# Optimization experiments

Measured on AMD Instinct MI355X. Metric: run time of the kernel, lower is better.

## Reference

```python
import jax, jax.numpy as jnp
import numpy as np

NUM_HEADS = 8
MASK_RATE = 0.5


def setup_inputs() -> dict:
    key = jax.random.key(0)
    ks = jax.random.split(key, 6)
    B, N, C = 8, 1024, 256
    TABLE = 10
    att_embedding = jax.random.normal(ks[0], (B, N, C), dtype=jnp.float32)
    relation_position = jax.random.randint(ks[1], (B, N, N), 0, TABLE, dtype=jnp.int32)
    rel_len = jax.random.randint(ks[2], (B,), 0, 20, dtype=jnp.int32)
    W_qkv = jax.random.normal(ks[3], (C, 3 * C), dtype=jnp.float32) * (1.0 / np.sqrt(C))
    W_proj = jax.random.normal(ks[4], (C, C), dtype=jnp.float32) * (1.0 / np.sqrt(C))
    b_proj = jnp.zeros((C,), dtype=jnp.float32)
    bias_table = jax.random.normal(ks[5], (TABLE, NUM_HEADS), dtype=jnp.float32) * 0.02
    return {
        "att_embedding": att_embedding,
        "relation_position": relation_position,
        "rel_len": rel_len,
        "W_qkv": W_qkv,
        "W_proj": W_proj,
        "b_proj": b_proj,
        "bias_table": bias_table,
    }


def reference(att_embedding, relation_position, rel_len, W_qkv, W_proj, b_proj, bias_table):
    B, N, C = att_embedding.shape
    H = NUM_HEADS
    hd = C // H
    scale = hd ** -0.5

    # QKV projection (no bias): [B,N,3C] -> q,k,v each [B,H,N,hd]
    qkv = (att_embedding @ W_qkv).reshape(B, N, 3, H, hd)
    qkv = jnp.transpose(qkv, (2, 0, 3, 1, 4))
    q, k, v = qkv[0], qkv[1], qkv[2]

    # Attention scores [B,H,N,N]
    attn = jnp.einsum("bhnd,bhmd->bhnm", q, k) * scale

    # Relative position bias: gather [B,N,N,H] -> [B,H,N,N]
    pos_bias = jnp.transpose(bias_table[relation_position], (0, 3, 1, 2))

    # Mask bias: table row t gets -100 iff t > mask_len (mask_len+1 .. TABLE-1);
    # identical across heads -> compute as [B,1,N,N] instead of materializing [B,H,N,N].
    mask_len = (rel_len.astype(jnp.float32) * MASK_RATE).astype(jnp.int32)
    mask_bias = jnp.where(relation_position > mask_len[:, None, None], -100.0, 0.0)[:, None]

    attn = jax.nn.softmax(attn + pos_bias + mask_bias, axis=-1)

    # Weighted values -> [B,N,C] -> output projection
    x = jnp.einsum("bhnm,bhmd->bnhd", attn, v).reshape(B, N, C)
    x = x @ W_proj + b_proj
    return x
```

## Files before the change

### kernel.cpp

```cpp
#include <hip/hip_runtime.h>
#include <hip/hip_bf16.h>

typedef __bf16 bf16;
typedef __bf16 bf16x2 __attribute__((ext_vector_type(2)));
typedef __bf16 bf16x8 __attribute__((ext_vector_type(8)));
typedef float f32x4 __attribute__((ext_vector_type(4)));
typedef int i32x4 __attribute__((ext_vector_type(4)));

#define B_ 8
#define N_ 1024
#define C_ 256
#define H_ 8
#define C3_ 768
#define SCALE 0.17677669529663689f
#define FMAX 16.0f


__global__ __launch_bounds__(256) void prep(
    const float* __restrict__ Wqkv, const float* __restrict__ Wproj,
    bf16* __restrict__ Wq_tiled, bf16* __restrict__ Wp_tiled)
{
  int bb = blockIdx.x;
  int o = bb * 256 + threadIdx.x;
  if (bb < 768) {
    int kk = o & 31;
    int idx = o >> 5;
    int nr = idx & 63;
    int qq = idx >> 6;
    int nt = qq % 12, kt = qq / 12;
    int n = nt * 64 + nr, k = kt * 32 + kk;
    Wq_tiled[o] = (bf16)Wqkv[k * C3_ + n];
  } else {
    int p = o - 768 * 256;
    int kk = p & 31;
    int n = (p >> 5) & 255;
    int kt = p >> 13;
    int k = kt * 32 + kk;
    Wp_tiled[p] = (bf16)Wproj[k * C_ + n];
  }
}

__global__ __launch_bounds__(256) void gemm_qkv(
    const float* __restrict__ A, const bf16* __restrict__ Wq_tiled,
    bf16* __restrict__ q, bf16* __restrict__ kT, bf16* __restrict__ vT)
{
  __shared__ bf16 As[128][40];
  __shared__ bf16 Bts[128][40];
  __shared__ bf16 Vls[64][136];

  int tid = threadIdx.x;
  int wave = tid >> 6, lane = tid & 63, quad = lane >> 4, l16 = lane & 15;
  int m0 = blockIdx.x * 128, n0 = blockIdx.y * 128;
  int msub = (wave & 1) * 64, nsub = (wave >> 1) * 64;

  f32x4 acc[4][4] = {};

  int arow = tid >> 1, akc = (tid & 1) * 16;
  const float* aptr = A + (long)(m0 + arow) * C_ + akc;
  int bn = tid >> 1, bkc = (tid & 1) * 16;
  const bf16* bptr = Wq_tiled +
      ((long)(blockIdx.y * 2 + (bn >> 6)) * 2048 + (bn & 63) * 32 + bkc);

  float4 a0 = *reinterpret_cast<const float4*>(aptr);
  float4 a1 = *reinterpret_cast<const float4*>(aptr + 4);
  float4 a2 = *reinterpret_cast<const float4*>(aptr + 8);
  float4 a3 = *reinterpret_cast<const float4*>(aptr + 12);
  i32x4 bv0 = *reinterpret_cast<const i32x4*>(bptr);
  i32x4 bv1 = *reinterpret_cast<const i32x4*>(bptr + 8);

  for (int kt = 0; kt < 8; ++kt) {
    __syncthreads();
    {
      bf16 at[16] = {(bf16)a0.x, (bf16)a0.y, (bf16)a0.z, (bf16)a0.w,
                     (bf16)a1.x, (bf16)a1.y, (bf16)a1.z, (bf16)a1.w,
                     (bf16)a2.x, (bf16)a2.y, (bf16)a2.z, (bf16)a2.w,
                     (bf16)a3.x, (bf16)a3.y, (bf16)a3.z, (bf16)a3.w};
      *reinterpret_cast<bf16x8*>(&As[arow][akc]) = *reinterpret_cast<bf16x8*>(at);
      *reinterpret_cast<bf16x8*>(&As[arow][akc + 8]) = *reinterpret_cast<bf16x8*>(at + 8);
      *reinterpret_cast<i32x4*>(&Bts[bn][bkc]) = bv0;
      *reinterpret_cast<i32x4*>(&Bts[bn][bkc + 8]) = bv1;
    }
    __syncthreads();

    if (kt < 7) {
      int kn = (kt + 1) * 32;
      a0 = *reinterpret_cast<const float4*>(aptr + kn);
      a1 = *reinterpret_cast<const float4*>(aptr + kn + 4);
      a2 = *reinterpret_cast<const float4*>(aptr + kn + 8);
      a3 = *reinterpret_cast<const float4*>(aptr + kn + 12);
      bv0 = *reinterpret_cast<const i32x4*>(bptr + (long)(kt + 1) * 24576);
      bv1 = *reinterpret_cast<const i32x4*>(bptr + (long)(kt + 1) * 24576 + 8);
    }

    bf16x8 af[4], bfr[4];
#pragma unroll
    for (int mi = 0; mi < 4; ++mi)
      af[mi] = *reinterpret_cast<const bf16x8*>(&As[msub + mi * 16 + l16][quad * 8]);
#pragma unroll
    for (int ni = 0; ni < 4; ++ni)
      bfr[ni] = *reinterpret_cast<const bf16x8*>(&Bts[nsub + ni * 16 + l16][quad * 8]);
#pragma unroll
    for (int mi = 0; mi < 4; ++mi)
#pragma unroll
      for (int ni = 0; ni < 4; ++ni)
        acc[mi][ni] = __builtin_amdgcn_mfma_f32_16x16x32_bf16(af[mi], bfr[ni], acc[mi][ni], 0, 0, 0);
  }

  if (n0 < 256) {
#pragma unroll
    for (int mi = 0; mi < 4; ++mi)
#pragma unroll
      for (int ni = 0; ni < 4; ++ni)
#pragma unroll
        for (int r = 0; r < 4; ++r) {
          int row = m0 + msub + mi * 16 + quad * 4 + r;
          int col = n0 + nsub + ni * 16 + l16;
          q[(long)row * 256 + col] = (bf16)(acc[mi][ni][r] * SCALE);
        }
  } else if (n0 < 512) {
#pragma unroll
    for (int mi = 0; mi < 4; ++mi)
#pragma unroll
      for (int ni = 0; ni < 4; ++ni)
#pragma unroll
        for (int r = 0; r < 4; ++r) {
          int row = m0 + msub + mi * 16 + quad * 4 + r;
          int c = n0 + nsub + ni * 16 + l16 - 256;
          int b = row >> 10, n = row & 1023;
          int h = c >> 5, d = c & 31;
          kT[(((long)(b * H_ + h)) * N_ + n) * 32 + d] = (bf16)acc[mi][ni][r];
        }
  } else {
    int b = m0 >> 10;
#pragma unroll
    for (int ch = 0; ch < 2; ++ch) {
      __syncthreads();
      if ((nsub >> 6) == ch) {
#pragma unroll
        for (int mi = 0; mi < 4; ++mi)
#pragma unroll
          for (int ni = 0; ni < 4; ++ni)
#pragma unroll
            for (int r = 0; r < 4; ++r) {
              int cc = ni * 16 + l16;
              int nn = msub + mi * 16 + quad * 4 + r;
              int np = (nn & 96) | (2 * (nn & 15)) | ((nn >> 4) & 1);
              Vls[cc][np] = (bf16)acc[mi][ni][r];
            }
      }
      __syncthreads();
      int cc = tid >> 2, nseg = (tid & 3) * 32;
      long base = ((long)(b * C_ + (n0 - 512) + ch * 64 + cc)) * N_ + (m0 & 1023) + nseg;
#pragma unroll
      for (int j = 0; j < 4; ++j)
        *reinterpret_cast<i32x4*>(vT + base + j * 8) =
            *reinterpret_cast<const i32x4*>(&Vls[cc][nseg + j * 8]);
    }
  }
}

__global__ __launch_bounds__(512) void flash_attn(
    const bf16* __restrict__ q, const bf16* __restrict__ kT,
    const bf16* __restrict__ vT, const int* __restrict__ rel,
    const int* __restrict__ rel_len, const float* __restrict__ btab,
    const bf16* __restrict__ Wp_tiled, const float* __restrict__ bias,
    float* __restrict__ out)
{
  __shared__ bf16 Pls[H_][16 * 40];
  __shared__ float btl[H_][16];
  __shared__ bf16 attL[16][264];

  int tid = threadIdx.x;
  int h = tid >> 6, lane = tid & 63, quad = lane >> 4, l16 = lane & 15;

  int wg = blockIdx.y * 64 + blockIdx.x;
  int swz = (wg & 7) * 64 + (wg >> 3);
  int b = swz >> 6, i0 = (swz & 63) * 16;
  long bN = (long)b * N_;

  int mask_len = (int)((float)rel_len[b] * 0.5f);
  if (tid < 80) {
    int t = tid >> 3, hh = tid & 7;
    btl[hh][t] = btab[t * H_ + hh] + (t > mask_len ? -100.f : 0.f) - FMAX;
  }
  __syncthreads();

  bf16x8 qf = *reinterpret_cast<const bf16x8*>(
      q + (bN + i0 + l16) * 256 + h * 32 + quad * 8);

  const bf16* kb_ = kT + ((long)(b * H_ + h)) * N_ * 32 + quad * 8;
  const bf16* vb_ = vT + ((long)b * C_ + h * 32 + l16) * N_ + quad * 8;
  const int*  rb_ = rel + (bN + i0 + quad * 4) * N_ + l16;

#define W_(J) ((J) < N_ ? (J) : 0)

#define LDK(K0, K1, V0, V1, J) do {                                          \
    K0 = *reinterpret_cast<const bf16x8*>(kb_ + (long)((J) + l16) * 32);     \
    K1 = *reinterpret_cast<const bf16x8*>(kb_ + (long)((J) + 16 + l16) * 32);\
    V0 = *reinterpret_cast<const bf16x8*>(vb_ + (J));                        \
    V1 = *reinterpret_cast<const bf16x8*>(vb_ + 16 * N_ + (J));              \
  } while (0)

#define LDR(RV, J) do {                                                      \
    _Pragma("unroll")                                                        \
    for (int r = 0; r < 4; ++r) {                                            \
      RV[2 * r]     = rb_[r * N_ + (J)];                                     \
      RV[2 * r + 1] = rb_[r * N_ + (J) + 16];                                \
    }                                                                        \
  } while (0)

#define COMP(K0, K1, V0, V1, RV) do {                                        \
    f32x4 z = {};                                                            \
    f32x4 s0 = __builtin_amdgcn_mfma_f32_16x16x32_bf16(qf, K0, z, 0, 0, 0);  \
    f32x4 s1 = __builtin_amdgcn_mfma_f32_16x16x32_bf16(qf, K1, z, 0, 0, 0);  \
    _Pragma("unroll")                                                        \
    for (int r = 0; r < 4; ++r) {                                            \
      float p0 = __expf(s0[r] + btl[h][RV[2 * r]]);                          \
      float p1 = __expf(s1[r] + btl[h][RV[2 * r + 1]]);                      \
      l_part[r] += p0 + p1;                                                  \
      bf16x2 pp = {(bf16)p0, (bf16)p1};    \
      *reinterpret_cast<bf16x2*>(&Pls[h][(quad * 4 + r) * 40 + l16 * 2]) = pp;\
    }                                                                        \
    asm volatile("s_waitcnt lgkmcnt(0)" ::: "memory");                       \
    bf16x8 pf = *reinterpret_cast<const bf16x8*>(&Pls[h][l16 * 40 + quad * 8]);\
    oacc[0] = __builtin_amdgcn_mfma_f32_16x16x32_bf16(pf, V0, oacc[0], 0, 0, 0);\
    oacc[1] = __builtin_amdgcn_mfma_f32_16x16x32_bf16(pf, V1, oacc[1], 0, 0, 0);\
  } while (0)

  f32x4 oacc[2] = {};
  float l_part[4] = {0.f, 0.f, 0.f, 0.f};

  bf16x8 ka0, ka1, vA0, vA1, kb0, kb1, vB0, vB1;
  int ra[8], rb2[8];

  LDK(ka0, ka1, vA0, vA1, 0);
  LDK(kb0, kb1, vB0, vB1, 32);
  LDR(ra, 0); LDR(rb2, 32);

#pragma unroll 1
  for (int j0 = 0; j0 < N_; j0 += 64) {
    COMP(ka0, ka1, vA0, vA1, ra);
    LDK(ka0, ka1, vA0, vA1, W_(j0 + 64));
    LDR(ra, W_(j0 + 64));
    COMP(kb0, kb1, vB0, vB1, rb2);
    LDK(kb0, kb1, vB0, vB1, W_(j0 + 96));
    LDR(rb2, W_(j0 + 96));
  }

#pragma unroll
  for (int r = 0; r < 4; ++r) {
    float l = l_part[r];
#pragma unroll
    for (int m = 1; m < 16; m <<= 1) l += __shfl_xor(l, m);
    float inv = 1.f / l;
    attL[quad * 4 + r][h * 32 + l16] = (bf16)(oacc[0][r] * inv);
    attL[quad * 4 + r][h * 32 + 16 + l16] = (bf16)(oacc[1][r] * inv);
  }
  __syncthreads();

  f32x4 pacc[2] = {};
  const bf16* wp = Wp_tiled + ((h * 32 + l16) * 32 + quad * 8);
#pragma unroll
  for (int kt = 0; kt < 8; ++kt) {
    bf16x8 afr = *reinterpret_cast<const bf16x8*>(&attL[l16][kt * 32 + quad * 8]);
    bf16x8 b0 = *reinterpret_cast<const bf16x8*>(wp + kt * 8192);
    bf16x8 b1 = *reinterpret_cast<const bf16x8*>(wp + kt * 8192 + 512);
    pacc[0] = __builtin_amdgcn_mfma_f32_16x16x32_bf16(afr, b0, pacc[0], 0, 0, 0);
    pacc[1] = __builtin_amdgcn_mfma_f32_16x16x32_bf16(afr, b1, pacc[1], 0, 0, 0);
  }
  float bi0 = bias[h * 32 + l16];
  float bi1 = bias[h * 32 + 16 + l16];
#pragma unroll
  for (int r = 0; r < 4; ++r) {
    long rowoff = (bN + i0 + quad * 4 + r) * C_ + h * 32;
    out[rowoff + l16] = pacc[0][r] + bi0;
    out[rowoff + 16 + l16] = pacc[1][r] + bi1;
  }
#undef W_
#undef LDK
#undef LDR
#undef COMP
}

extern "C" void kernel_launch(void* const* d_in, const int* in_sizes, int n_in,
                              void* d_out, int out_size, void* d_ws, size_t ws_size,
                              hipStream_t stream) {
  const float* X     = (const float*)d_in[0];
  const int*   rel   = (const int*)d_in[1];
  const int*   rlen  = (const int*)d_in[2];
  const float* Wqkv  = (const float*)d_in[3];
  const float* Wproj = (const float*)d_in[4];
  const float* bproj = (const float*)d_in[5];
  const float* btab  = (const float*)d_in[6];
  float* out = (float*)d_out;

  char* ws = (char*)d_ws;
  bf16* Wq_tiled = (bf16*)ws;
  bf16* Wp_tiled = (bf16*)(ws + 393216);
  bf16* q  = (bf16*)(ws + 524288);
  bf16* kT = (bf16*)(ws + 524288 + 4194304);
  bf16* vT = (bf16*)(ws + 524288 + 2 * 4194304);

  prep<<<dim3(1024), 256, 0, stream>>>(Wqkv, Wproj, Wq_tiled, Wp_tiled);
  gemm_qkv<<<dim3(8192 / 128, C3_ / 128), 256, 0, stream>>>(X, Wq_tiled, q, kT, vT);
  flash_attn<<<dim3(N_ / 16, B_), 512, 0, stream>>>(
      q, kT, vT, rel, rlen, btab, Wp_tiled, bproj, out);
}
```

Baseline: 160.5 us.

## Compute S transposed to keep P in registers and drop LDS round-trip

```diff
diff --git a/kernel.cpp b/kernel.cpp
--- a/kernel.cpp
+++ b/kernel.cpp
@@ -144,7 +144,7 @@
             for (int r = 0; r < 4; ++r) {
               int cc = ni * 16 + l16;
               int nn = msub + mi * 16 + quad * 4 + r;
-              int np = (nn & 96) | (2 * (nn & 15)) | ((nn >> 4) & 1);
+              int np = (nn & 96) | ((nn & 12) << 1) | (nn & 3) | (((nn >> 4) & 1) << 2);
               Vls[cc][np] = (bf16)acc[mi][ni][r];
             }
       }
@@ -166,8 +166,7 @@
     const bf16* __restrict__ Wp_tiled, const float* __restrict__ bias,
     float* __restrict__ out)
 {
-  __shared__ bf16 Pls[H_][16 * 40];
-  __shared__ float btl[H_][16];
+  __shared__ float ebtl[H_][16];
   __shared__ bf16 attL[16][264];
 
   int tid = threadIdx.x;
@@ -181,7 +180,7 @@
   int mask_len = (int)((float)rel_len[b] * 0.5f);
   if (tid < 80) {
     int t = tid >> 3, hh = tid & 7;
-    btl[hh][t] = btab[t * H_ + hh] + (t > mask_len ? -100.f : 0.f) - FMAX;
+    ebtl[hh][t] = __expf(btab[t * H_ + hh] + (t > mask_len ? -100.f : 0.f) - FMAX);
   }
   __syncthreads();
 
@@ -190,71 +189,85 @@
 
   const bf16* kb_ = kT + ((long)(b * H_ + h)) * N_ * 32 + quad * 8;
   const bf16* vb_ = vT + ((long)b * C_ + h * 32 + l16) * N_ + quad * 8;
-  const int*  rb_ = rel + (bN + i0 + quad * 4) * N_ + l16;
+  const int*  rb_ = rel + (bN + i0 + l16) * N_ + quad * 4;
+
+  f32x4 oacc[2] = {};
+  float l_acc = 0.f;
 
 #define W_(J) ((J) < N_ ? (J) : 0)
 
-#define LDK(K0, K1, V0, V1, J) do {                                          \
+#define LD_KV(K0, K1, V0, V1, J) do {                                        \
     K0 = *reinterpret_cast<const bf16x8*>(kb_ + (long)((J) + l16) * 32);     \
     K1 = *reinterpret_cast<const bf16x8*>(kb_ + (long)((J) + 16 + l16) * 32);\
     V0 = *reinterpret_cast<const bf16x8*>(vb_ + (J));                        \
     V1 = *reinterpret_cast<const bf16x8*>(vb_ + 16 * N_ + (J));              \
   } while (0)
 
-#define LDR(RV, J) do {                                                      \
+#define LD_R(R0, R1, J) do {                                                 \
+    R0 = *reinterpret_cast<const i32x4*>(rb_ + (J));                         \
+    R1 = *reinterpret_cast<const i32x4*>(rb_ + (J) + 16);                    \
+  } while (0)
+
+#define GATH(G, R0, R1) do {                                                 \
     _Pragma("unroll")                                                        \
-    for (int r = 0; r < 4; ++r) {                                            \
-      RV[2 * r]     = rb_[r * N_ + (J)];                                     \
-      RV[2 * r + 1] = rb_[r * N_ + (J) + 16];                                \
+    for (int e = 0; e < 4; ++e) {                                            \
+      G[e]     = ebtl[h][R0[e]];                                             \
+      G[4 + e] = ebtl[h][R1[e]];                                             \
     }                                                                        \
   } while (0)
 
-#define COMP(K0, K1, V0, V1, RV) do {                                        \
+#define COMP(K0, K1, V0, V1, G) do {                                         \
     f32x4 z = {};                                                            \
-    f32x4 s0 = __builtin_amdgcn_mfma_f32_16x16x32_bf16(qf, K0, z, 0, 0, 0);  \
-    f32x4 s1 = __builtin_amdgcn_mfma_f32_16x16x32_bf16(qf, K1, z, 0, 0, 0);  \
+    f32x4 s0 = __builtin_amdgcn_mfma_f32_16x16x32_bf16(K0, qf, z, 0, 0, 0);  \
+    f32x4 s1 = __builtin_amdgcn_mfma_f32_16x16x32_bf16(K1, qf, z, 0, 0, 0);  \
+    bf16x8 pa;                                                               \
     _Pragma("unroll")                                                        \
-    for (int r = 0; r < 4; ++r) {                                            \
-      float p0 = __expf(s0[r] + btl[h][RV[2 * r]]);                          \
-      float p1 = __expf(s1[r] + btl[h][RV[2 * r + 1]]);                      \
-      l_part[r] += p0 + p1;                                                  \
-      bf16x2 pp = {(bf16)p0, (bf16)p1};    \
-      *reinterpret_cast<bf16x2*>(&Pls[h][(quad * 4 + r) * 40 + l16 * 2]) = pp;\
+    for (int e = 0; e < 4; ++e) {                                            \
+      float p0 = __expf(s0[e]) * G[e];                                       \
+      float p1 = __expf(s1[e]) * G[4 + e];                                   \
+      l_acc += p0 + p1;                                                      \
+      pa[e] = (bf16)p0;                                                      \
+      pa[4 + e] = (bf16)p1;                                                  \
     }                                                                        \
-    asm volatile("s_waitcnt lgkmcnt(0)" ::: "memory");                       \
-    bf16x8 pf = *reinterpret_cast<const bf16x8*>(&Pls[h][l16 * 40 + quad * 8]);\
-    oacc[0] = __builtin_amdgcn_mfma_f32_16x16x32_bf16(pf, V0, oacc[0], 0, 0, 0);\
-    oacc[1] = __builtin_amdgcn_mfma_f32_16x16x32_bf16(pf, V1, oacc[1], 0, 0, 0);\
+    oacc[0] = __builtin_amdgcn_mfma_f32_16x16x32_bf16(pa, V0, oacc[0], 0, 0, 0); \
+    oacc[1] = __builtin_amdgcn_mfma_f32_16x16x32_bf16(pa, V1, oacc[1], 0, 0, 0); \
   } while (0)
 
-  f32x4 oacc[2] = {};
-  float l_part[4] = {0.f, 0.f, 0.f, 0.f};
-
-  bf16x8 ka0, ka1, vA0, vA1, kb0, kb1, vB0, vB1;
-  int ra[8], rb2[8];
-
-  LDK(ka0, ka1, vA0, vA1, 0);
-  LDK(kb0, kb1, vB0, vB1, 32);
-  LDR(ra, 0); LDR(rb2, 32);
+  bf16x8 kX0, kX1, vX0, vX1, kY0, kY1, vY0, vY1;
+  i32x4 rX0, rX1, rY0, rY1;
+  float gX[8], gY[8];
+
+  LD_KV(kX0, kX1, vX0, vX1, 0);  LD_R(rX0, rX1, 0);
+  LD_KV(kY0, kY1, vY0, vY1, 32); LD_R(rY0, rY1, 32);
+  GATH(gX, rX0, rX1);
 
 #pragma unroll 1
   for (int j0 = 0; j0 < N_; j0 += 64) {
-    COMP(ka0, ka1, vA0, vA1, ra);
-    LDK(ka0, ka1, vA0, vA1, W_(j0 + 64));
-    LDR(ra, W_(j0 + 64));
-    COMP(kb0, kb1, vB0, vB1, rb2);
-    LDK(kb0, kb1, vB0, vB1, W_(j0 + 96));
-    LDR(rb2, W_(j0 + 96));
-  }
+    GATH(gY, rY0, rY1);
+    COMP(kX0, kX1, vX0, vX1, gX);
+    LD_KV(kX0, kX1, vX0, vX1, W_(j0 + 64));
+    LD_R(rX0, rX1, W_(j0 + 64));
+    GATH(gX, rX0, rX1);
+    COMP(kY0, kY1, vY0, vY1, gY);
+    LD_KV(kY0, kY1, vY0, vY1, W_(j0 + 96));
+    LD_R(rY0, rY1, W_(j0 + 96));
+  }
+#undef COMP
+#undef GATH
+#undef LD_R
+#undef LD_KV
+#undef W_
+
+  float lsum = l_acc;
+  lsum += __shfl_xor(lsum, 16);
+  lsum += __shfl_xor(lsum, 32);
+  float inv = 1.f / lsum;
 
 #pragma unroll
   for (int r = 0; r < 4; ++r) {
-    float l = l_part[r];
-#pragma unroll
-    for (int m = 1; m < 16; m <<= 1) l += __shfl_xor(l, m);
-    float inv = 1.f / l;
-    attL[quad * 4 + r][h * 32 + l16] = (bf16)(oacc[0][r] * inv);
-    attL[quad * 4 + r][h * 32 + 16 + l16] = (bf16)(oacc[1][r] * inv);
+    float invr = __shfl(inv, quad * 4 + r);
+    attL[quad * 4 + r][h * 32 + l16] = (bf16)(oacc[0][r] * invr);
+    attL[quad * 4 + r][h * 32 + 16 + l16] = (bf16)(oacc[1][r] * invr);
   }
   __syncthreads();
 
@@ -276,10 +289,6 @@
     out[rowoff + l16] = pacc[0][r] + bi0;
     out[rowoff + 16 + l16] = pacc[1][r] + bi1;
   }
-#undef W_
-#undef LDK
-#undef LDR
-#undef COMP
 }
 
 extern "C" void kernel_launch(void* const* d_in, const int* in_sizes, int n_in,
```

New measurement: 176.3 us. +9.9%, slower.
